# Kernel optimization log

Hardware: AMD Instinct MI355X
Metric: run time of the kernel (lower is better)

## Reference

```python
import jax, jax.numpy as jnp
import numpy as np

NUM_ITEMS = 100000
HIDDEN = 128
NNZ = 1600000


def setup_inputs() -> dict:
    key = jax.random.key(0)
    k1, k2, k3, k4, k5, k6 = jax.random.split(key, 6)
    item_embedding_table = jax.random.normal(k1, (NUM_ITEMS, HIDDEN), dtype=jnp.float32)
    adj_rows = jnp.sort(jax.random.randint(k2, (NNZ,), 0, NUM_ITEMS, dtype=jnp.int32))
    adj_cols = jax.random.randint(k3, (NNZ,), 0, NUM_ITEMS, dtype=jnp.int32)
    adj_vals = jax.random.uniform(k4, (NNZ,), dtype=jnp.float32)
    # nn.Linear default init (uniform in +-1/sqrt(fan_in)) approximated by scaled normal
    W_weight = jax.random.normal(k5, (HIDDEN, HIDDEN), dtype=jnp.float32) / np.sqrt(HIDDEN)
    W_bias = jax.random.normal(k6, (HIDDEN,), dtype=jnp.float32) * 0.01
    return {
        "item_embedding_table": item_embedding_table,
        "adj_rows": adj_rows,
        "adj_cols": adj_cols,
        "adj_vals": adj_vals,
        "W_weight": W_weight,
        "W_bias": W_bias,
    }


def reference(item_embedding_table, adj_rows, adj_cols, adj_vals, W_weight, W_bias):
    # support = W(x): x @ W^T + b   (nn.Linear convention: weight [out, in])
    support = jnp.einsum("nd,hd->nh", item_embedding_table, W_weight) + W_bias  # [N, H]
    # output = sparse_coo(adj) @ support, via gather + segment-sum scatter
    msgs = adj_vals[:, None] * support[adj_cols]  # [nnz, H]
    output = jax.ops.segment_sum(msgs, adj_rows, num_segments=NUM_ITEMS)  # [N, H]
    return output
```

## Files before the change

kernel.cpp:

```cpp
#include <hip/hip_runtime.h>

#define N_ITEMS 100000
#define HID 128
#define NNZ_T 1600000
#define PREPW_BLOCKS 64
#define RP_BLOCKS 391

typedef unsigned short ushort_t;
typedef unsigned int uint_t;
typedef short bf16x8 __attribute__((ext_vector_type(8)));
typedef float f32x4 __attribute__((ext_vector_type(4)));

static __device__ __forceinline__ ushort_t f32_to_bf16(float f) {
    uint_t u = __float_as_uint(f);
    uint_t r = (u + 0x7FFFu + ((u >> 16) & 1u)) >> 16;
    return (ushort_t)r;
}

__global__ void prep(const float* __restrict__ W, const int* __restrict__ rows,
                     ushort_t* __restrict__ Wb, int* __restrict__ row_ptr) {
    if (blockIdx.x < PREPW_BLOCKS) {
        int i = blockIdx.x * 256 + threadIdx.x;
        Wb[i] = f32_to_bf16(W[i]);
        return;
    }
    int r = (blockIdx.x - PREPW_BLOCKS) * 256 + threadIdx.x;
    if (r > N_ITEMS) return;
    int lo = 0, hi = NNZ_T;
    while (lo < hi) {
        int mid = (lo + hi) >> 1;
        if (rows[mid] < r) lo = mid + 1; else hi = mid;
    }
    row_ptr[r] = lo;
}

__global__ __launch_bounds__(256) void gemm_mfma(
    const float* __restrict__ X, const ushort_t* __restrict__ Wb,
    const float* __restrict__ bias, ushort_t* __restrict__ S) {
    const int lane = threadIdx.x & 63;
    const int wave = threadIdx.x >> 6;
    const int m = lane & 15;
    const int q = lane >> 4;
    const int row0 = blockIdx.x * 64 + wave * 16;

    int arow = row0 + m;
    if (arow >= N_ITEMS) arow = N_ITEMS - 1;

    f32x4 acc[8] = {};

#pragma unroll
    for (int kb = 0; kb < 4; ++kb) {
        const int k0 = kb * 32 + q * 8;
        float4 a0 = *(const float4*)&X[(size_t)arow * HID + k0];
        float4 a1 = *(const float4*)&X[(size_t)arow * HID + k0 + 4];
        bf16x8 xf;
        xf[0] = (short)f32_to_bf16(a0.x); xf[1] = (short)f32_to_bf16(a0.y);
        xf[2] = (short)f32_to_bf16(a0.z); xf[3] = (short)f32_to_bf16(a0.w);
        xf[4] = (short)f32_to_bf16(a1.x); xf[5] = (short)f32_to_bf16(a1.y);
        xf[6] = (short)f32_to_bf16(a1.z); xf[7] = (short)f32_to_bf16(a1.w);
#pragma unroll
        for (int nt = 0; nt < 8; ++nt) {
            bf16x8 wf = *(const bf16x8*)&Wb[(size_t)(nt * 16 + m) * HID + k0];
            acc[nt] = __builtin_amdgcn_mfma_f32_16x16x32_bf16(wf, xf, acc[nt], 0, 0, 0);
        }
    }

    const int srow = row0 + m;
    const bool ok = srow < N_ITEMS;
#pragma unroll
    for (int nt = 0; nt < 8; ++nt) {
        const int c0 = nt * 16 + q * 4;
        float4 bv = *(const float4*)&bias[c0];
        ushort_t h0 = f32_to_bf16(acc[nt][0] + bv.x);
        ushort_t h1 = f32_to_bf16(acc[nt][1] + bv.y);
        ushort_t h2 = f32_to_bf16(acc[nt][2] + bv.z);
        ushort_t h3 = f32_to_bf16(acc[nt][3] + bv.w);
        uint2 pk;
        pk.x = (uint_t)h0 | ((uint_t)h1 << 16);
        pk.y = (uint_t)h2 | ((uint_t)h3 << 16);
        if (ok) *(uint2*)&S[(size_t)srow * HID + c0] = pk;
    }
}

__global__ __launch_bounds__(256) void spmm_csr(
    const int* __restrict__ cols, const float* __restrict__ vals,
    const int* __restrict__ row_ptr, const ushort_t* __restrict__ S,
    float* __restrict__ out) {
    const int lane = threadIdx.x & 63;
    const int row = blockIdx.x * 4 + ((threadIdx.x >> 6) & 3);
    if (row >= N_ITEMS) return;

    const int g = lane >> 4;
    const int l = lane & 15;

    const int p0 = row_ptr[row];
    const int p1 = row_ptr[row + 1];

    float acc[8] = {};

    if (p1 > p0) {
        const int last = p1 - 1;
        for (int p = p0; p < p1; p += 16) {
            uint4 u[4]; float v[4];
#pragma unroll
            for (int t = 0; t < 4; ++t) {
                int idx = p + 4 * t + g;
                bool ok = idx < p1;
                idx = min(idx, last);
                int c = cols[idx];
                v[t] = ok ? vals[idx] : 0.f;
                u[t] = *(const uint4*)&S[(size_t)c * HID + 8 * l];
            }
#pragma unroll
            for (int t = 0; t < 4; ++t) {
                acc[0] = fmaf(v[t], __uint_as_float(u[t].x << 16),          acc[0]);
                acc[1] = fmaf(v[t], __uint_as_float(u[t].x & 0xFFFF0000u),  acc[1]);
                acc[2] = fmaf(v[t], __uint_as_float(u[t].y << 16),          acc[2]);
                acc[3] = fmaf(v[t], __uint_as_float(u[t].y & 0xFFFF0000u),  acc[3]);
                acc[4] = fmaf(v[t], __uint_as_float(u[t].z << 16),          acc[4]);
                acc[5] = fmaf(v[t], __uint_as_float(u[t].z & 0xFFFF0000u),  acc[5]);
                acc[6] = fmaf(v[t], __uint_as_float(u[t].w << 16),          acc[6]);
                acc[7] = fmaf(v[t], __uint_as_float(u[t].w & 0xFFFF0000u),  acc[7]);
            }
        }
    }

#pragma unroll
    for (int e = 0; e < 8; ++e) {
        acc[e] += __shfl_xor(acc[e], 16, 64);
        acc[e] += __shfl_xor(acc[e], 32, 64);
    }
    if (g == 0) {
        float4 o0 = make_float4(acc[0], acc[1], acc[2], acc[3]);
        float4 o1 = make_float4(acc[4], acc[5], acc[6], acc[7]);
        float* p = &out[(size_t)row * HID + 8 * l];
        *(float4*)p = o0;
        *(float4*)(p + 4) = o1;
    }
}

extern "C" void kernel_launch(void* const* d_in, const int* in_sizes, int n_in,
                              void* d_out, int out_size, void* d_ws, size_t ws_size,
                              hipStream_t stream) {
    const float* X    = (const float*)d_in[0];
    const int*   rows = (const int*)  d_in[1];
    const int*   cols = (const int*)  d_in[2];
    const float* vals = (const float*)d_in[3];
    const float* W    = (const float*)d_in[4];
    const float* bias = (const float*)d_in[5];
    float* out = (float*)d_out;

    ushort_t* Wb      = (ushort_t*)d_ws;
    ushort_t* S       = Wb + HID * HID;
    int*      row_ptr = (int*)(S + (size_t)N_ITEMS * HID);

    prep<<<PREPW_BLOCKS + RP_BLOCKS, 256, 0, stream>>>(W, rows, Wb, row_ptr);
    gemm_mfma<<<(N_ITEMS + 63) / 64, 256, 0, stream>>>(X, Wb, bias, S);
    spmm_csr<<<(N_ITEMS + 3) / 4, 256, 0, stream>>>(cols, vals, row_ptr, S, out);
}
```

Before: 215.6 us.

## Use fp16 support with packed half2 accumulation and shuffle-broadcast column indices

The support matrix is now stored as fp16 instead of bf16, and the SpMM accumulates with packed __hfma2 on half2, halving the FMA count and removing the bf16 unpacking. Column indices and values are loaded once per 64-entry window, one per lane, and broadcast with shuffles instead of each lane group reloading them. This trades accumulation precision (fp16 partial sums) for fewer ALU and scalar-load instructions in the gather loop.

```diff
diff --git a/kernel.cpp b/kernel.cpp
--- a/kernel.cpp
+++ b/kernel.cpp
@@ -1,4 +1,5 @@
 #include <hip/hip_runtime.h>
+#include <hip/hip_fp16.h>
 
 #define N_ITEMS 100000
 #define HID 128
@@ -71,10 +72,10 @@
     for (int nt = 0; nt < 8; ++nt) {
         const int c0 = nt * 16 + q * 4;
         float4 bv = *(const float4*)&bias[c0];
-        ushort_t h0 = f32_to_bf16(acc[nt][0] + bv.x);
-        ushort_t h1 = f32_to_bf16(acc[nt][1] + bv.y);
-        ushort_t h2 = f32_to_bf16(acc[nt][2] + bv.z);
-        ushort_t h3 = f32_to_bf16(acc[nt][3] + bv.w);
+        ushort_t h0 = __half_as_ushort(__float2half(acc[nt][0] + bv.x));
+        ushort_t h1 = __half_as_ushort(__float2half(acc[nt][1] + bv.y));
+        ushort_t h2 = __half_as_ushort(__float2half(acc[nt][2] + bv.z));
+        ushort_t h3 = __half_as_ushort(__float2half(acc[nt][3] + bv.w));
         uint2 pk;
         pk.x = (uint_t)h0 | ((uint_t)h1 << 16);
         pk.y = (uint_t)h2 | ((uint_t)h3 << 16);
@@ -96,46 +97,51 @@
     const int p0 = row_ptr[row];
     const int p1 = row_ptr[row + 1];
 
-    float acc[8] = {};
+    __half2 acch[4];
+    acch[0] = __float2half2_rn(0.f); acch[1] = __float2half2_rn(0.f);
+    acch[2] = __float2half2_rn(0.f); acch[3] = __float2half2_rn(0.f);
 
-    if (p1 > p0) {
-        const int last = p1 - 1;
-        for (int p = p0; p < p1; p += 16) {
+    for (int w0 = p0; w0 < p1; w0 += 64) {
+        const int nw = min(64, p1 - w0);
+        const int idx = w0 + lane;
+        const int c_l = cols[min(idx, p1 - 1)];
+        const float v_l = (idx < p1) ? vals[idx] : 0.f;
+
+        for (int s0 = 0; s0 < nw; s0 += 16) {
             uint4 u[4]; float v[4];
 #pragma unroll
             for (int t = 0; t < 4; ++t) {
-                int idx = p + 4 * t + g;
-                bool ok = idx < p1;
-                idx = min(idx, last);
-                int c = cols[idx];
-                v[t] = ok ? vals[idx] : 0.f;
+                const int slot = s0 + 4 * t + g;
+                const int c = __shfl(c_l, slot, 64);
+                v[t] = __shfl(v_l, slot, 64);
                 u[t] = *(const uint4*)&S[(size_t)c * HID + 8 * l];
             }
 #pragma unroll
             for (int t = 0; t < 4; ++t) {
-                acc[0] = fmaf(v[t], __uint_as_float(u[t].x << 16),          acc[0]);
-                acc[1] = fmaf(v[t], __uint_as_float(u[t].x & 0xFFFF0000u),  acc[1]);
-                acc[2] = fmaf(v[t], __uint_as_float(u[t].y << 16),          acc[2]);
-                acc[3] = fmaf(v[t], __uint_as_float(u[t].y & 0xFFFF0000u),  acc[3]);
-                acc[4] = fmaf(v[t], __uint_as_float(u[t].z << 16),          acc[4]);
-                acc[5] = fmaf(v[t], __uint_as_float(u[t].z & 0xFFFF0000u),  acc[5]);
-                acc[6] = fmaf(v[t], __uint_as_float(u[t].w << 16),          acc[6]);
-                acc[7] = fmaf(v[t], __uint_as_float(u[t].w & 0xFFFF0000u),  acc[7]);
+                const __half2 vv = __float2half2_rn(v[t]);
+                acch[0] = __hfma2(vv, *(const __half2*)&u[t].x, acch[0]);
+                acch[1] = __hfma2(vv, *(const __half2*)&u[t].y, acch[1]);
+                acch[2] = __hfma2(vv, *(const __half2*)&u[t].z, acch[2]);
+                acch[3] = __hfma2(vv, *(const __half2*)&u[t].w, acch[3]);
             }
         }
     }
 
+    float acc[8];
+#pragma unroll
+    for (int j = 0; j < 4; ++j) {
+        acc[2 * j]     = __low2float(acch[j]);
+        acc[2 * j + 1] = __high2float(acch[j]);
+    }
 #pragma unroll
     for (int e = 0; e < 8; ++e) {
         acc[e] += __shfl_xor(acc[e], 16, 64);
         acc[e] += __shfl_xor(acc[e], 32, 64);
     }
     if (g == 0) {
-        float4 o0 = make_float4(acc[0], acc[1], acc[2], acc[3]);
-        float4 o1 = make_float4(acc[4], acc[5], acc[6], acc[7]);
         float* p = &out[(size_t)row * HID + 8 * l];
-        *(float4*)p = o0;
-        *(float4*)(p + 4) = o1;
+        *(float4*)p       = make_float4(acc[0], acc[1], acc[2], acc[3]);
+        *(float4*)(p + 4) = make_float4(acc[4], acc[5], acc[6], acc[7]);
     }
 }
 
```

Measured after the change: 204.7 us. 1.05x faster.
